# Kernel tuning notes

Hardware: AMD Instinct MI355X
Metric: run time of the kernel (lower is better)

Reference implementation:

```python
import jax, jax.numpy as jnp
import numpy as np
import math

R, C, B, E = 64, 256, 1, 768
H, DK, F = 8, 96, 3072
EPS = 1e-5


def _ln(x, w, b):
    m = jnp.mean(x, axis=-1, keepdims=True)
    v = jnp.var(x, axis=-1, keepdims=True)
    return (x - m) / jnp.sqrt(v + EPS) * w + b


def _lin(x, w, b):
    # torch Linear: y = x @ W^T + b, W: [out, in]
    return jnp.einsum('...i,oi->...o', x, w) + b


def setup_inputs() -> dict:
    key = jax.random.key(0)
    ks = jax.random.split(key, 16)
    w = lambda k, s: jax.random.normal(k, s, dtype=jnp.float32) * 0.02
    z = lambda s: jnp.zeros(s, dtype=jnp.float32)
    o = lambda s: jnp.ones(s, dtype=jnp.float32)
    return {
        'x': jax.random.normal(ks[0], (R, C, B, E), dtype=jnp.float32),
        'ln_row_w': o((E,)), 'ln_row_b': z((E,)),
        'row_q_w': w(ks[1], (E, E)), 'row_q_b': z((E,)),
        'row_k_w': w(ks[2], (E, E)), 'row_k_b': z((E,)),
        'row_v_w': w(ks[3], (E, E)), 'row_v_b': z((E,)),
        'row_o_w': w(ks[4], (E, E)), 'row_o_b': z((E,)),
        'ln_col_w': o((E,)), 'ln_col_b': z((E,)),
        'col_q_w': w(ks[5], (E, E)), 'col_q_b': z((E,)),
        'col_k_w': w(ks[6], (E, E)), 'col_k_b': z((E,)),
        'col_v_w': w(ks[7], (E, E)), 'col_v_b': z((E,)),
        'col_o_w': w(ks[8], (E, E)), 'col_o_b': z((E,)),
        'ln_ffn_w': o((E,)), 'ln_ffn_b': z((E,)),
        'fc1_w': w(ks[9], (F, E)), 'fc1_b': z((F,)),
        'fc2_w': w(ks[10], (E, F)), 'fc2_b': z((E,)),
    }


def reference(x, ln_row_w, ln_row_b, row_q_w, row_q_b, row_k_w, row_k_b,
              row_v_w, row_v_b, row_o_w, row_o_b,
              ln_col_w, ln_col_b, col_q_w, col_q_b, col_k_w, col_k_b,
              col_v_w, col_v_b, col_o_w, col_o_b,
              ln_ffn_w, ln_ffn_b, fc1_w, fc1_b, fc2_w, fc2_b):
    r, c, n, e = x.shape  # n_rows, n_cols, batch, embed

    # ---- Row self-attention (pre-LN residual block) ----
    xn = _ln(x, ln_row_w, ln_row_b)
    scaling = (DK ** -0.5) / math.sqrt(r)  # align_scaling: extra 1/sqrt(n_rows)
    q = _lin(xn, row_q_w, row_q_b).reshape(r, c, n, H, DK) * scaling
    k = _lin(xn, row_k_w, row_k_b).reshape(r, c, n, H, DK)
    v = _lin(xn, row_v_w, row_v_b).reshape(r, c, n, H, DK)
    row_logits = jnp.einsum('rinhd,rjnhd->hnij', q, k)  # sums over rows
    row_probs = jax.nn.softmax(row_logits, axis=-1)     # [H, B, C, C]
    rc = jnp.einsum('hnij,rjnhd->rinhd', row_probs, v).reshape(r, c, n, e)
    x = x + _lin(rc, row_o_w, row_o_b)

    # ---- Column self-attention (pre-LN residual block) ----
    xn = _ln(x, ln_col_w, ln_col_b)
    q = _lin(xn, col_q_w, col_q_b).reshape(r, c, n, H, DK) * (DK ** -0.5)
    k = _lin(xn, col_k_w, col_k_b).reshape(r, c, n, H, DK)
    v = _lin(xn, col_v_w, col_v_b).reshape(r, c, n, H, DK)
    col_logits = jnp.einsum('icnhd,jcnhd->hcnij', q, k)
    col_probs = jax.nn.softmax(col_logits, axis=-1)     # [H, C, B, R, R]
    cc = jnp.einsum('hcnij,jcnhd->icnhd', col_probs, v).reshape(r, c, n, e)
    x = x + _lin(cc, col_o_w, col_o_b)

    # ---- Feed-forward (pre-LN residual block) ----
    xn = _ln(x, ln_ffn_w, ln_ffn_b)
    h = jax.nn.gelu(_lin(xn, fc1_w, fc1_b), approximate=False)
    x = x + _lin(h, fc2_w, fc2_b)

    return x, row_probs, col_probs
```

## Files before the change

### kernel.cpp

```cpp
#include <hip/hip_runtime.h>
#include <cstdint>

typedef unsigned short u16;
typedef __attribute__((ext_vector_type(8))) short short8;
typedef __attribute__((ext_vector_type(4))) short short4v;
typedef __attribute__((ext_vector_type(4))) float floatx4;

#define DEV __device__ __forceinline__

DEV float bf2f(u16 u) { union { uint32_t i; float f; } w; w.i = ((uint32_t)u) << 16; return w.f; }
DEV u16 f2bf(float f) {
  union { float f; uint32_t i; } w; w.f = f;
  uint32_t x = w.i;
  return (u16)((x + 0x7fffu + ((x >> 16) & 1u)) >> 16);
}

DEV float fast_gelu(float x) {
  const float y = x * 0.70710678118f;
  const float ay = fabsf(y);
  const float t = 1.f / (1.f + 0.3275911f * ay);
  const float poly = t * (0.254829592f + t * (-0.284496736f +
                     t * (1.421413741f + t * (-1.453152027f + t * 1.061405429f))));
  const float er = 1.f - poly * __expf(-y * y);
  const float erf_y = __builtin_copysignf(er, y);
  return 0.5f * x * (1.f + erf_y);
}

DEV void async_copy16(const u16* g, u16* l) {
  __builtin_amdgcn_global_load_lds(
      (const __attribute__((address_space(1))) void*)(uintptr_t)g,
      (__attribute__((address_space(3))) void*)(uint32_t)(uintptr_t)l,
      16, 0, 0);
}

struct CvtArgs {
  const float* src[10];
  float scale[10];
};
__global__ __launch_bounds__(256) void cvt_all(CvtArgs a, u16* __restrict__ dst) {
  const size_t e = ((size_t)blockIdx.x * 256 + threadIdx.x) * 4;
  if (e >= 9437184) return;
  int reg;
  size_t base;
  if (e < 4718592) { reg = (int)(e / 589824); base = (size_t)reg * 589824; }
  else if (e < 7077888) { reg = 8; base = 4718592; }
  else { reg = 9; base = 7077888; }
  const float sc = a.scale[reg];
  floatx4 f = *(const floatx4*)(a.src[reg] + (e - base));
  short4v o;
#pragma unroll
  for (int j = 0; j < 4; ++j) o[j] = (short)f2bf(f[j] * sc);
  *(short4v*)(dst + e) = o;
}

__global__ __launch_bounds__(256) void bias_pack(const float* __restrict__ qb,
                                                 const float* __restrict__ kb,
                                                 const float* __restrict__ vb,
                                                 float sq, float* __restrict__ out) {
  const int i = blockIdx.x * 256 + threadIdx.x;
  if (i >= 2304) return;
  const int buf = i / 768, c = i - buf * 768;
  out[i] = buf == 0 ? qb[c] * sq : (buf == 1 ? kb[c] : vb[c]);
}

template<bool INF32>
__global__ __launch_bounds__(256) void ln_kernel(const void* __restrict__ in,
                                                 const float* __restrict__ w,
                                                 const float* __restrict__ b,
                                                 u16* __restrict__ out) {
  const int wid = threadIdx.x >> 6, lane = threadIdx.x & 63;
  const int row = blockIdx.x * 4 + wid;
  const size_t base = (size_t)row * 768;
  float v[12];
#pragma unroll
  for (int p = 0; p < 3; ++p) {
    const int e = p * 256 + lane * 4;
    if constexpr (INF32) {
      floatx4 f = *(const floatx4*)((const float*)in + base + e);
#pragma unroll
      for (int j = 0; j < 4; ++j) v[p * 4 + j] = f[j];
    } else {
      short4v u = *(const short4v*)((const u16*)in + base + e);
#pragma unroll
      for (int j = 0; j < 4; ++j) v[p * 4 + j] = bf2f((u16)u[j]);
    }
  }
  float s = 0.f, sq = 0.f;
#pragma unroll
  for (int i = 0; i < 12; ++i) { s += v[i]; sq += v[i] * v[i]; }
#pragma unroll
  for (int m = 1; m < 64; m <<= 1) { s += __shfl_xor(s, m); sq += __shfl_xor(sq, m); }
  const float mean = s * (1.f / 768.f);
  const float var = sq * (1.f / 768.f) - mean * mean;
  const float rstd = rsqrtf(var + 1e-5f);
#pragma unroll
  for (int p = 0; p < 3; ++p) {
    const int e = p * 256 + lane * 4;
    floatx4 wv = *(const floatx4*)(w + e);
    floatx4 bv = *(const floatx4*)(b + e);
    short4v o;
#pragma unroll
    for (int j = 0; j < 4; ++j) {
      float y = (v[p * 4 + j] - mean) * rstd * wv[j] + bv[j];
      o[j] = (short)f2bf(y);
    }
    *(short4v*)(out + base + e) = o;
  }
}

template<int AMODE>
DEV void stage_tile(const u16* __restrict__ Ab, const u16* __restrict__ Bb,
                    int m0, int n0, int lda, int ldb, int kk0, int t,
                    u16* ldsA, u16* ldsB) {
  const int wid = t >> 6;
  const int col = (((t & 3) ^ ((t >> 2) & 3)) << 3);
#pragma unroll
  for (int i = 0; i < 2; ++i) {
    const int r = i * 64 + (t >> 2);
    const int kk = kk0 + col;
    const u16 *ga, *gb;
    if constexpr (AMODE == 0) {
      ga = Ab + (size_t)(m0 + r) * lda + kk;
      gb = Bb + (size_t)(n0 + r) * ldb + kk;
    } else {
      const int r96 = kk / 96, d = kk - r96 * 96;
      ga = Ab + (size_t)r96 * 196608 + (size_t)(m0 + r) * 768 + d;
      gb = Bb + (size_t)r96 * 196608 + (size_t)(n0 + r) * 768 + d;
    }
    async_copy16(ga, ldsA + i * 2048 + wid * 512);
    async_copy16(gb, ldsB + i * 2048 + wid * 512);
  }
}

template<int AMODE, int EPI>
__global__ __launch_bounds__(256) void gemm_bt(
    const u16* __restrict__ A, const u16* __restrict__ B,
    const float* __restrict__ bias, const void* __restrict__ res,
    void* __restrict__ out, int K, int lda, int ldb,
    long long aBatch, long long bBatch, long long outBatch, int ldc, float scale) {
  __shared__ u16 lds[3 * 8192];
  const int t = threadIdx.x;
  const int z = blockIdx.z;
  const int m0 = blockIdx.x * 128, n0 = blockIdx.y * 128;
  const u16* Ab;
  const u16* Bb;
  int koff = 0;
  if constexpr (AMODE == 0) { Ab = A + (size_t)z * aBatch; Bb = B + (size_t)z * bBatch; }
  else if constexpr (AMODE == 1) { Ab = A + z * 96; Bb = B + z * 96; }
  else { const int h = z >> 4; Ab = A + h * 96; Bb = B + h * 96; koff = (z & 15) * 384; }

  const int wid = t >> 6, lane = t & 63;
  const int wr = wid >> 1, wc = wid & 1;
  const int lrow = lane & 15, lhi = lane >> 4;
  const int swl = lrow & 3;

  floatx4 acc[4][4];
#pragma unroll
  for (int i = 0; i < 4; ++i)
#pragma unroll
    for (int j = 0; j < 4; ++j) acc[i][j] = (floatx4){0.f, 0.f, 0.f, 0.f};

  const int NT = K >> 5;

  stage_tile<AMODE>(Ab, Bb, m0, n0, lda, ldb, koff, t, lds, lds + 4096);
  if (NT > 1)
    stage_tile<AMODE>(Ab, Bb, m0, n0, lda, ldb, koff + 32, t, lds + 8192, lds + 8192 + 4096);
  if (NT > 2) asm volatile("s_waitcnt vmcnt(4)" ::: "memory");
  else        asm volatile("s_waitcnt vmcnt(0)" ::: "memory");
  __builtin_amdgcn_s_barrier();
  asm volatile("" ::: "memory");

  int cur = 0, nxt = 2;
  for (int kt = 0; kt < NT; ++kt) {
    const bool more = (kt + 2) < NT;
    if (more)
      stage_tile<AMODE>(Ab, Bb, m0, n0, lda, ldb, koff + (kt + 2) * 32, t,
                        lds + nxt * 8192, lds + nxt * 8192 + 4096);

    const u16* lA = lds + cur * 8192;
    const u16* lB = lA + 4096;
    short8 af[4], bfr[4];
#pragma unroll
    for (int mi = 0; mi < 4; ++mi)
      af[mi] = *(const short8*)&lA[(wr * 64 + mi * 16 + lrow) * 32 + ((lhi ^ swl) << 3)];
#pragma unroll
    for (int ni = 0; ni < 4; ++ni)
      bfr[ni] = *(const short8*)&lB[(wc * 64 + ni * 16 + lrow) * 32 + ((lhi ^ swl) << 3)];

    __builtin_amdgcn_s_setprio(1);
#pragma unroll
    for (int mi = 0; mi < 4; ++mi)
#pragma unroll
      for (int ni = 0; ni < 4; ++ni)
        acc[mi][ni] = __builtin_amdgcn_mfma_f32_16x16x32_bf16(af[mi], bfr[ni], acc[mi][ni], 0, 0, 0);
    __builtin_amdgcn_s_setprio(0);

    if (kt + 1 < NT) {
      if (more) asm volatile("s_waitcnt vmcnt(4)" ::: "memory");
      else      asm volatile("s_waitcnt vmcnt(0)" ::: "memory");
      __builtin_amdgcn_s_barrier();
      asm volatile("" ::: "memory");
    }
    cur = (cur == 2) ? 0 : cur + 1;
    nxt = (nxt == 2) ? 0 : nxt + 1;
  }

  const int mbase = m0 + wr * 64;
  const int nbase = n0 + wc * 64;
#pragma unroll
  for (int mi = 0; mi < 4; ++mi) {
#pragma unroll
    for (int ni = 0; ni < 4; ++ni) {
      const int n = nbase + ni * 16 + lrow;
      float bz = 0.f;
      if constexpr (EPI != 1 && EPI != 7) { if (bias) bz = bias[n]; }
#pragma unroll
      for (int r4 = 0; r4 < 4; ++r4) {
        const int m = mbase + mi * 16 + lhi * 4 + r4;
        const float val = acc[mi][ni][r4];
        if constexpr (EPI == 1) {
          ((float*)out)[(size_t)z * outBatch + (size_t)m * ldc + n] = val;
        } else if constexpr (EPI == 2) {
          ((u16*)out)[(size_t)m * ldc + n] = f2bf(fast_gelu(val + bz));
        } else if constexpr (EPI == 3) {
          const float r = ((const float*)res)[(size_t)m * ldc + n];
          ((float*)out)[(size_t)m * ldc + n] = r + val + bz;
        } else if constexpr (EPI == 4) {
          const float r = ((const float*)res)[(size_t)m * ldc + n];
          ((u16*)out)[(size_t)m * ldc + n] = f2bf(r + val + bz);
        } else if constexpr (EPI == 5) {
          const float r = bf2f(((const u16*)res)[(size_t)m * ldc + n]);
          ((float*)out)[(size_t)m * ldc + n] = r + val + bz;
        } else if constexpr (EPI == 6) {
          const float r = bf2f(((const u16*)res)[(size_t)m * ldc + n]);
          ((u16*)out)[(size_t)m * ldc + n] = f2bf(r + val + bz);
        } else if constexpr (EPI == 7) {
          const int rr = n / 96, d = n - rr * 96;
          ((u16*)out)[((size_t)(rr * 256 + m)) * 768 + (size_t)z * 96 + d] = f2bf(val);
        } else if constexpr (EPI == 8) {
          const int buf = n / 768, col = n - buf * 768;
          ((u16*)out)[(size_t)buf * 12582912 + (size_t)m * 768 + col] = f2bf(val + bz);
        }
      }
    }
  }
}

__global__ __launch_bounds__(256) void softmax_row(const float* __restrict__ part,
                                                   float* __restrict__ probs_f,
                                                   u16* __restrict__ probs_b) {
  const int wid = threadIdx.x >> 6, lane = threadIdx.x & 63;
  const int row = blockIdx.x * 4 + wid;
  const int h = row >> 8, i = row & 255;
  const size_t base = (size_t)h * 16 * 65536 + (size_t)i * 256 + lane * 4;
  floatx4 v = (floatx4){0.f, 0.f, 0.f, 0.f};
#pragma unroll
  for (int s16 = 0; s16 < 16; ++s16) {
    floatx4 p = *(const floatx4*)(part + base + (size_t)s16 * 65536);
#pragma unroll
    for (int j = 0; j < 4; ++j) v[j] += p[j];
  }
  float mx = fmaxf(fmaxf(v[0], v[1]), fmaxf(v[2], v[3]));
#pragma unroll
  for (int m = 1; m < 64; m <<= 1) mx = fmaxf(mx, __shfl_xor(mx, m));
  float e[4], s = 0.f;
#pragma unroll
  for (int j = 0; j < 4; ++j) { e[j] = __expf(v[j] - mx); s += e[j]; }
#pragma unroll
  for (int m = 1; m < 64; m <<= 1) s += __shfl_xor(s, m);
  const float inv = 1.f / s;
  floatx4 of;
  short4v ob;
#pragma unroll
  for (int j = 0; j < 4; ++j) {
    const float p = e[j] * inv;
    of[j] = p;
    ob[j] = (short)f2bf(p);
  }
  *(floatx4*)(probs_f + (size_t)row * 256 + lane * 4) = of;
  *(short4v*)(probs_b + (size_t)row * 256 + lane * 4) = ob;
}

__global__ __launch_bounds__(256) void pack_vt(const u16* __restrict__ v, u16* __restrict__ vt) {
  __shared__ u16 S[64][104];
  const int jb = blockIdx.x, r = blockIdx.y, h = blockIdx.z;
  const int t = threadIdx.x;
#pragma unroll
  for (int p = 0; p < 3; ++p) {
    const int cid = t + p * 256;
    const int j = cid / 12, ch = cid - j * 12;
    short8 x = *(const short8*)&v[((size_t)(r * 256 + jb * 64 + j)) * 768 + h * 96 + ch * 8];
    *(short8*)&S[j][ch * 8] = x;
  }
  __syncthreads();
#pragma unroll
  for (int p = 0; p < 3; ++p) {
    const int cid = t + p * 256;
    const int d = cid / 8, cj = cid - d * 8;
    u16 tmp[8];
#pragma unroll
    for (int m = 0; m < 8; ++m) tmp[m] = S[cj * 8 + m][d];
    *(short8*)&vt[((size_t)(h * 6144 + r * 96 + d)) * 256 + jb * 64 + cj * 8] = *(short8*)tmp;
  }
}

__global__ __launch_bounds__(256) void col_attn(const u16* __restrict__ q,
                                                const u16* __restrict__ k,
                                                const u16* __restrict__ v,
                                                float* __restrict__ probs,
                                                u16* __restrict__ ctx) {
  __shared__ u16 qs[64][104];
  __shared__ u16 ks[64][104];
  __shared__ u16 vt[96][72];
  __shared__ u16 ps[64][72];
  const int c = blockIdx.x, h = blockIdx.y;
  const int t = threadIdx.x;
#pragma unroll
  for (int p = 0; p < 3; ++p) {
    const int cid = t + p * 256;
    const int i = cid / 12, ch = cid - i * 12;
    const size_t g = ((size_t)(i * 256 + c)) * 768 + h * 96 + ch * 8;
    short8 qv = *(const short8*)(q + g);
    short8 kv = *(const short8*)(k + g);
    short8 vv = *(const short8*)(v + g);
    *(short8*)&qs[i][ch * 8] = qv;
    *(short8*)&ks[i][ch * 8] = kv;
#pragma unroll
    for (int m = 0; m < 8; ++m) vt[ch * 8 + m][i] = (u16)vv[m];
  }
  __syncthreads();
  const int lane = t & 63, wid = t >> 6;
  const int lrow = lane & 15, lhi = lane >> 4;

  floatx4 s[4];
#pragma unroll
  for (int nj = 0; nj < 4; ++nj) s[nj] = (floatx4){0.f, 0.f, 0.f, 0.f};
#pragma unroll
  for (int kk = 0; kk < 3; ++kk) {
    short8 a = *(const short8*)&qs[wid * 16 + lrow][kk * 32 + lhi * 8];
#pragma unroll
    for (int nj = 0; nj < 4; ++nj) {
      short8 bb = *(const short8*)&ks[nj * 16 + lrow][kk * 32 + lhi * 8];
      s[nj] = __builtin_amdgcn_mfma_f32_16x16x32_bf16(a, bb, s[nj], 0, 0, 0);
    }
  }
  const size_t pb = ((size_t)(h * 256 + c)) * 4096;
#pragma unroll
  for (int r4 = 0; r4 < 4; ++r4) {
    float mx = fmaxf(fmaxf(s[0][r4], s[1][r4]), fmaxf(s[2][r4], s[3][r4]));
    mx = fmaxf(mx, __shfl_xor(mx, 1));
    mx = fmaxf(mx, __shfl_xor(mx, 2));
    mx = fmaxf(mx, __shfl_xor(mx, 4));
    mx = fmaxf(mx, __shfl_xor(mx, 8));
    float e[4], sum = 0.f;
#pragma unroll
    for (int nj = 0; nj < 4; ++nj) { e[nj] = __expf(s[nj][r4] - mx); sum += e[nj]; }
    sum += __shfl_xor(sum, 1);
    sum += __shfl_xor(sum, 2);
    sum += __shfl_xor(sum, 4);
    sum += __shfl_xor(sum, 8);
    const float inv = 1.f / sum;
    const int i = wid * 16 + lhi * 4 + r4;
#pragma unroll
    for (int nj = 0; nj < 4; ++nj) {
      const float pv = e[nj] * inv;
      const int j = nj * 16 + lrow;
      probs[pb + (size_t)i * 64 + j] = pv;
      ps[i][j] = f2bf(pv);
    }
  }
  __syncthreads();
  floatx4 o[6];
#pragma unroll
  for (int df = 0; df < 6; ++df) o[df] = (floatx4){0.f, 0.f, 0.f, 0.f};
#pragma unroll
  for (int k2 = 0; k2 < 2; ++k2) {
    short8 a = *(const short8*)&ps[wid * 16 + lrow][k2 * 32 + lhi * 8];
#pragma unroll
    for (int df = 0; df < 6; ++df) {
      short8 bb = *(const short8*)&vt[df * 16 + lrow][k2 * 32 + lhi * 8];
      o[df] = __builtin_amdgcn_mfma_f32_16x16x32_bf16(a, bb, o[df], 0, 0, 0);
    }
  }
#pragma unroll
  for (int df = 0; df < 6; ++df)
#pragma unroll
    for (int r4 = 0; r4 < 4; ++r4) {
      const int i = wid * 16 + lhi * 4 + r4;
      const int d = df * 16 + lrow;
      ctx[((size_t)(i * 256 + c)) * 768 + h * 96 + d] = f2bf(o[df][r4]);
    }
}

extern "C" void kernel_launch(void* const* d_in, const int* in_sizes, int n_in,
                              void* d_out, int out_size, void* d_ws, size_t ws_size,
                              hipStream_t stream) {
  const float* x_in  = (const float*)d_in[0];
  const float* lnr_w = (const float*)d_in[1];
  const float* lnr_b = (const float*)d_in[2];
  const float* rq_w  = (const float*)d_in[3];
  const float* rq_b  = (const float*)d_in[4];
  const float* rk_w  = (const float*)d_in[5];
  const float* rk_b  = (const float*)d_in[6];
  const float* rv_w  = (const float*)d_in[7];
  const float* rv_b  = (const float*)d_in[8];
  const float* ro_w  = (const float*)d_in[9];
  const float* ro_b  = (const float*)d_in[10];
  const float* lnc_w = (const float*)d_in[11];
  const float* lnc_b = (const float*)d_in[12];
  const float* cq_w  = (const float*)d_in[13];
  const float* cq_b  = (const float*)d_in[14];
  const float* ck_w  = (const float*)d_in[15];
  const float* ck_b  = (const float*)d_in[16];
  const float* cv_w  = (const float*)d_in[17];
  const float* cv_b  = (const float*)d_in[18];
  const float* co_w  = (const float*)d_in[19];
  const float* co_b  = (const float*)d_in[20];
  const float* lnf_w = (const float*)d_in[21];
  const float* lnf_b = (const float*)d_in[22];
  const float* f1_w  = (const float*)d_in[23];
  const float* f1_b  = (const float*)d_in[24];
  const float* f2_w  = (const float*)d_in[25];
  const float* f2_b  = (const float*)d_in[26];

  const float s_row = 0.0127577591f;
  const float s_col = 0.1020620726f;

  char* ws = (char*)d_ws;
  const size_t WSZ_E = 589824 * 2;
  u16* w_all = (u16*)ws;
  u16* w_rqkv = w_all;
  u16* w_ro   = (u16*)(ws + 3 * WSZ_E);
  u16* w_cqkv = (u16*)(ws + 4 * WSZ_E);
  u16* w_co   = (u16*)(ws + 7 * WSZ_E);
  u16* w_f1   = (u16*)(ws + 8 * WSZ_E);
  u16* w_f2   = (u16*)(ws + 8 * WSZ_E + 4718592);
  size_t off = 8 * WSZ_E + 2 * 4718592;

  const bool xf32 = ws_size >= 147849216ULL;
  char* x_cur = ws + off;
  off += xf32 ? 50331648 : 25165824;
  u16* qb = (u16*)(ws + off); off += 25165824;
  u16* kb = (u16*)(ws + off); off += 25165824;
  u16* vb = (u16*)(ws + off); off += 25165824;
  u16* probsb = (u16*)(ws + off); off += 1048576;
  float* qkvb_row = (float*)(ws + off); off += 9216;
  float* qkvb_col = (float*)(ws + off); off += 9216;

  u16* vt     = qb;
  u16* ctx1   = kb;
  u16* hidden = qb;
  u16* xn3    = vb;

  float* out_x  = (float*)d_out;
  float* out_rp = out_x + 12582912;
  float* out_cp = out_x + 13107200;
  u16* xn   = (u16*)out_x;
  u16* ctx2 = (u16*)((char*)out_x + 25165824);
  float* part = out_x;

  const dim3 blk(256);

  CvtArgs ca;
  ca.src[0] = rq_w; ca.src[1] = rk_w; ca.src[2] = rv_w; ca.src[3] = ro_w;
  ca.src[4] = cq_w; ca.src[5] = ck_w; ca.src[6] = cv_w; ca.src[7] = co_w;
  ca.src[8] = f1_w; ca.src[9] = f2_w;
  for (int i = 0; i < 10; ++i) ca.scale[i] = 1.f;
  ca.scale[0] = s_row; ca.scale[4] = s_col;
  cvt_all<<<9216, blk, 0, stream>>>(ca, w_all);
  bias_pack<<<9, blk, 0, stream>>>(rq_b, rk_b, rv_b, s_row, qkvb_row);
  bias_pack<<<9, blk, 0, stream>>>(cq_b, ck_b, cv_b, s_col, qkvb_col);

  ln_kernel<true><<<4096, blk, 0, stream>>>(x_in, lnr_w, lnr_b, xn);
  gemm_bt<0, 8><<<dim3(128, 18, 1), blk, 0, stream>>>(xn, w_rqkv, qkvb_row, nullptr, qb, 768, 768, 768, 0, 0, 0, 768, 1.f);
  gemm_bt<2, 1><<<dim3(2, 2, 128), blk, 0, stream>>>(qb, kb, nullptr, nullptr, part, 384, 0, 0, 0, 0, 65536LL, 256, 1.f);
  softmax_row<<<512, blk, 0, stream>>>(part, out_rp, probsb);
  pack_vt<<<dim3(4, 64, 8), blk, 0, stream>>>(vb, vt);
  gemm_bt<0, 7><<<dim3(2, 48, 8), blk, 0, stream>>>(probsb, vt, nullptr, nullptr, ctx1, 256, 256, 256, 65536LL, 1572864LL, 0, 0, 1.f);
  if (xf32)
    gemm_bt<0, 3><<<dim3(128, 6, 1), blk, 0, stream>>>(ctx1, w_ro, ro_b, x_in, x_cur, 768, 768, 768, 0, 0, 0, 768, 1.f);
  else
    gemm_bt<0, 4><<<dim3(128, 6, 1), blk, 0, stream>>>(ctx1, w_ro, ro_b, x_in, x_cur, 768, 768, 768, 0, 0, 0, 768, 1.f);

  if (xf32) ln_kernel<true><<<4096, blk, 0, stream>>>(x_cur, lnc_w, lnc_b, xn);
  else      ln_kernel<false><<<4096, blk, 0, stream>>>(x_cur, lnc_w, lnc_b, xn);
  gemm_bt<0, 8><<<dim3(128, 18, 1), blk, 0, stream>>>(xn, w_cqkv, qkvb_col, nullptr, qb, 768, 768, 768, 0, 0, 0, 768, 1.f);
  col_attn<<<dim3(256, 8), blk, 0, stream>>>(qb, kb, vb, out_cp, ctx2);
  if (xf32)
    gemm_bt<0, 3><<<dim3(128, 6, 1), blk, 0, stream>>>(ctx2, w_co, co_b, x_cur, x_cur, 768, 768, 768, 0, 0, 0, 768, 1.f);
  else
    gemm_bt<0, 6><<<dim3(128, 6, 1), blk, 0, stream>>>(ctx2, w_co, co_b, x_cur, x_cur, 768, 768, 768, 0, 0, 0, 768, 1.f);

  if (xf32) ln_kernel<true><<<4096, blk, 0, stream>>>(x_cur, lnf_w, lnf_b, xn3);
  else      ln_kernel<false><<<4096, blk, 0, stream>>>(x_cur, lnf_w, lnf_b, xn3);
  gemm_bt<0, 2><<<dim3(128, 12, 1), blk, 0, stream>>>(xn3, w_f1, f1_b, nullptr, hidden, 768, 768, 768, 0, 0, 0, 1536, 1.f);
  if (xf32)
    gemm_bt<0, 3><<<dim3(128, 6, 1), blk, 0, stream>>>(hidden, w_f2, f2_b, x_cur, out_x, 1536, 1536, 3072, 0, 0, 0, 768, 1.f);
  else
    gemm_bt<0, 5><<<dim3(128, 6, 1), blk, 0, stream>>>(hidden, w_f2, f2_b, x_cur, out_x, 1536, 1536, 3072, 0, 0, 0, 768, 1.f);
  gemm_bt<0, 2><<<dim3(128, 12, 1), blk, 0, stream>>>(xn3, w_f1 + 1536 * 768, f1_b + 1536, nullptr, hidden, 768, 768, 768, 0, 0, 0, 1536, 1.f);
  gemm_bt<0, 3><<<dim3(128, 6, 1), blk, 0, stream>>>(hidden, w_f2 + 1536, nullptr, out_x, out_x, 1536, 1536, 3072, 0, 0, 0, 768, 1.f);
}
```

Measured before the change: 620.1 us.

## Pre-pack GEMM B operands into tile-contiguous layout for coalesced LDS staging

Weights and the transposed V buffer are now written in a blocked layout of 128x32 tiles, with the 8-element k-chunks laid out contiguously. The GEMM gains a BP template mode that stages B with one fully contiguous 16-byte load per lane and reads fragments without swizzling. The goal is better global-load coalescing and fewer LDS bank conflicts on the B side. In exchange, the weight conversion kernel now reads with a strided gather, and the ldb argument is reinterpreted as a count of k-tiles per row.

Result: no change. 618.9 us (-0.2%).

```diff
diff --git a/kernel.cpp b/kernel.cpp
--- a/kernel.cpp
+++ b/kernel.cpp
@@ -40,16 +40,23 @@
 __global__ __launch_bounds__(256) void cvt_all(CvtArgs a, u16* __restrict__ dst) {
   const size_t e = ((size_t)blockIdx.x * 256 + threadIdx.x) * 4;
   if (e >= 9437184) return;
-  int reg;
+  int reg, N, K;
   size_t base;
-  if (e < 4718592) { reg = (int)(e / 589824); base = (size_t)reg * 589824; }
-  else if (e < 7077888) { reg = 8; base = 4718592; }
-  else { reg = 9; base = 7077888; }
+  if (e < 4718592) { reg = (int)(e / 589824); base = (size_t)reg * 589824; N = 768; K = 768; }
+  else if (e < 7077888) { reg = 8; base = 4718592; N = 3072; K = 768; }
+  else { reg = 9; base = 7077888; N = 768; K = 3072; }
+  const int NKT = K >> 5;
+  const size_t r = e - base;
+  const int tile = (int)(r >> 12);
+  const int nt = tile / NKT, kt = tile - nt * NKT;
+  const int rem = (int)(r & 4095);
+  const int c = rem >> 10, row = (rem >> 3) & 127, j = rem & 7;
+  const int n = nt * 128 + row, k = kt * 32 + c * 8 + j;
   const float sc = a.scale[reg];
-  floatx4 f = *(const floatx4*)(a.src[reg] + (e - base));
+  floatx4 f = *(const floatx4*)(a.src[reg] + (size_t)n * K + k);
   short4v o;
 #pragma unroll
-  for (int j = 0; j < 4; ++j) o[j] = (short)f2bf(f[j] * sc);
+  for (int q = 0; q < 4; ++q) o[q] = (short)f2bf(f[q] * sc);
   *(short4v*)(dst + e) = o;
 }
 
@@ -108,36 +115,49 @@
   }
 }
 
-template<int AMODE>
-DEV void stage_tile(const u16* __restrict__ Ab, const u16* __restrict__ Bb,
-                    int m0, int n0, int lda, int ldb, int kk0, int t,
+template<int AMODE, int BP>
+DEV void stage_tile(const u16* __restrict__ Ab, const u16* __restrict__ Bsrc,
+                    int m0, int n0, int lda, int ldb, int kk0, int ktAbs, int t,
                     u16* ldsA, u16* ldsB) {
-  const int wid = t >> 6;
+  const int wid = t >> 6, lane = t & 63;
   const int col = (((t & 3) ^ ((t >> 2) & 3)) << 3);
 #pragma unroll
   for (int i = 0; i < 2; ++i) {
     const int r = i * 64 + (t >> 2);
     const int kk = kk0 + col;
-    const u16 *ga, *gb;
+    const u16* ga;
     if constexpr (AMODE == 0) {
       ga = Ab + (size_t)(m0 + r) * lda + kk;
-      gb = Bb + (size_t)(n0 + r) * ldb + kk;
     } else {
       const int r96 = kk / 96, d = kk - r96 * 96;
       ga = Ab + (size_t)r96 * 196608 + (size_t)(m0 + r) * 768 + d;
-      gb = Bb + (size_t)r96 * 196608 + (size_t)(n0 + r) * 768 + d;
     }
     async_copy16(ga, ldsA + i * 2048 + wid * 512);
-    async_copy16(gb, ldsB + i * 2048 + wid * 512);
-  }
-}
-
-template<int AMODE, int EPI>
+
+    const int slot = i * 4 + wid;
+    if constexpr (BP) {
+      const u16* gb = Bsrc + (size_t)ktAbs * 4096 + slot * 512 + lane * 8;
+      async_copy16(gb, ldsB + slot * 512);
+    } else {
+      const u16* gb;
+      if constexpr (AMODE == 0) {
+        gb = Bsrc + (size_t)(n0 + r) * ldb + kk;
+      } else {
+        const int r96 = kk / 96, d = kk - r96 * 96;
+        gb = Bsrc + (size_t)r96 * 196608 + (size_t)(n0 + r) * 768 + d;
+      }
+      async_copy16(gb, ldsB + i * 2048 + wid * 512);
+    }
+  }
+}
+
+template<int AMODE, int EPI, int BP>
 __global__ __launch_bounds__(256) void gemm_bt(
     const u16* __restrict__ A, const u16* __restrict__ B,
     const float* __restrict__ bias, const void* __restrict__ res,
     void* __restrict__ out, int K, int lda, int ldb,
-    long long aBatch, long long bBatch, long long outBatch, int ldc, float scale) {
+    long long aBatch, long long bBatch, long long outBatch, int ldc, int bkt0,
+    float scale) {
   __shared__ u16 lds[3 * 8192];
   const int t = threadIdx.x;
   const int z = blockIdx.z;
@@ -146,8 +166,11 @@
   const u16* Bb;
   int koff = 0;
   if constexpr (AMODE == 0) { Ab = A + (size_t)z * aBatch; Bb = B + (size_t)z * bBatch; }
-  else if constexpr (AMODE == 1) { Ab = A + z * 96; Bb = B + z * 96; }
   else { const int h = z >> 4; Ab = A + h * 96; Bb = B + h * 96; koff = (z & 15) * 384; }
+
+  const u16* Bstage;
+  if constexpr (BP) Bstage = Bb + ((size_t)((n0 >> 7) * ldb + bkt0)) * 4096;
+  else Bstage = Bb;
 
   const int wid = t >> 6, lane = t & 63;
   const int wr = wid >> 1, wc = wid & 1;
@@ -162,9 +185,10 @@
 
   const int NT = K >> 5;
 
-  stage_tile<AMODE>(Ab, Bb, m0, n0, lda, ldb, koff, t, lds, lds + 4096);
+  stage_tile<AMODE, BP>(Ab, Bstage, m0, n0, lda, ldb, koff, 0, t, lds, lds + 4096);
   if (NT > 1)
-    stage_tile<AMODE>(Ab, Bb, m0, n0, lda, ldb, koff + 32, t, lds + 8192, lds + 8192 + 4096);
+    stage_tile<AMODE, BP>(Ab, Bstage, m0, n0, lda, ldb, koff + 32, 1, t,
+                          lds + 8192, lds + 8192 + 4096);
   if (NT > 2) asm volatile("s_waitcnt vmcnt(4)" ::: "memory");
   else        asm volatile("s_waitcnt vmcnt(0)" ::: "memory");
   __builtin_amdgcn_s_barrier();
@@ -174,8 +198,8 @@
   for (int kt = 0; kt < NT; ++kt) {
     const bool more = (kt + 2) < NT;
     if (more)
-      stage_tile<AMODE>(Ab, Bb, m0, n0, lda, ldb, koff + (kt + 2) * 32, t,
-                        lds + nxt * 8192, lds + nxt * 8192 + 4096);
+      stage_tile<AMODE, BP>(Ab, Bstage, m0, n0, lda, ldb, koff + (kt + 2) * 32, kt + 2, t,
+                            lds + nxt * 8192, lds + nxt * 8192 + 4096);
 
     const u16* lA = lds + cur * 8192;
     const u16* lB = lA + 4096;
@@ -184,8 +208,12 @@
     for (int mi = 0; mi < 4; ++mi)
       af[mi] = *(const short8*)&lA[(wr * 64 + mi * 16 + lrow) * 32 + ((lhi ^ swl) << 3)];
 #pragma unroll
-    for (int ni = 0; ni < 4; ++ni)
-      bfr[ni] = *(const short8*)&lB[(wc * 64 + ni * 16 + lrow) * 32 + ((lhi ^ swl) << 3)];
+    for (int ni = 0; ni < 4; ++ni) {
+      if constexpr (BP)
+        bfr[ni] = *(const short8*)&lB[lhi * 1024 + (wc * 64 + ni * 16 + lrow) * 8];
+      else
+        bfr[ni] = *(const short8*)&lB[(wc * 64 + ni * 16 + lrow) * 32 + ((lhi ^ swl) << 3)];
+    }
 
     __builtin_amdgcn_s_setprio(1);
 #pragma unroll
@@ -300,7 +328,12 @@
     u16 tmp[8];
 #pragma unroll
     for (int m = 0; m < 8; ++m) tmp[m] = S[cj * 8 + m][d];
-    *(short8*)&vt[((size_t)(h * 6144 + r * 96 + d)) * 256 + jb * 64 + cj * 8] = *(short8*)tmp;
+    const int row_t = r * 96 + d;
+    const int k = jb * 64 + cj * 8;
+    const size_t off = (size_t)h * 1572864 +
+                       ((size_t)((row_t >> 7) * 8 + (k >> 5))) * 4096 +
+                       ((k >> 3) & 3) * 1024 + (row_t & 127) * 8;
+    *(short8*)&vt[off] = *(short8*)tmp;
   }
 }
 
@@ -472,32 +505,32 @@
   bias_pack<<<9, blk, 0, stream>>>(cq_b, ck_b, cv_b, s_col, qkvb_col);
 
   ln_kernel<true><<<4096, blk, 0, stream>>>(x_in, lnr_w, lnr_b, xn);
-  gemm_bt<0, 8><<<dim3(128, 18, 1), blk, 0, stream>>>(xn, w_rqkv, qkvb_row, nullptr, qb, 768, 768, 768, 0, 0, 0, 768, 1.f);
-  gemm_bt<2, 1><<<dim3(2, 2, 128), blk, 0, stream>>>(qb, kb, nullptr, nullptr, part, 384, 0, 0, 0, 0, 65536LL, 256, 1.f);
+  gemm_bt<0, 8, 1><<<dim3(128, 18, 1), blk, 0, stream>>>(xn, w_rqkv, qkvb_row, nullptr, qb, 768, 768, 24, 0, 0, 0, 768, 0, 1.f);
+  gemm_bt<2, 1, 0><<<dim3(2, 2, 128), blk, 0, stream>>>(qb, kb, nullptr, nullptr, part, 384, 0, 0, 0, 0, 65536LL, 256, 0, 1.f);
   softmax_row<<<512, blk, 0, stream>>>(part, out_rp, probsb);
   pack_vt<<<dim3(4, 64, 8), blk, 0, stream>>>(vb, vt);
-  gemm_bt<0, 7><<<dim3(2, 48, 8), blk, 0, stream>>>(probsb, vt, nullptr, nullptr, ctx1, 256, 256, 256, 65536LL, 1572864LL, 0, 0, 1.f);
+  gemm_bt<0, 7, 1><<<dim3(2, 48, 8), blk, 0, stream>>>(probsb, vt, nullptr, nullptr, ctx1, 256, 256, 8, 65536LL, 1572864LL, 0, 0, 0, 1.f);
   if (xf32)
-    gemm_bt<0, 3><<<dim3(128, 6, 1), blk, 0, stream>>>(ctx1, w_ro, ro_b, x_in, x_cur, 768, 768, 768, 0, 0, 0, 768, 1.f);
+    gemm_bt<0, 3, 1><<<dim3(128, 6, 1), blk, 0, stream>>>(ctx1, w_ro, ro_b, x_in, x_cur, 768, 768, 24, 0, 0, 0, 768, 0, 1.f);
   else
-    gemm_bt<0, 4><<<dim3(128, 6, 1), blk, 0, stream>>>(ctx1, w_ro, ro_b, x_in, x_cur, 768, 768, 768, 0, 0, 0, 768, 1.f);
+    gemm_bt<0, 4, 1><<<dim3(128, 6, 1), blk, 0, stream>>>(ctx1, w_ro, ro_b, x_in, x_cur, 768, 768, 24, 0, 0, 0, 768, 0, 1.f);
 
   if (xf32) ln_kernel<true><<<4096, blk, 0, stream>>>(x_cur, lnc_w, lnc_b, xn);
   else      ln_kernel<false><<<4096, blk, 0, stream>>>(x_cur, lnc_w, lnc_b, xn);
-  gemm_bt<0, 8><<<dim3(128, 18, 1), blk, 0, stream>>>(xn, w_cqkv, qkvb_col, nullptr, qb, 768, 768, 768, 0, 0, 0, 768, 1.f);
+  gemm_bt<0, 8, 1><<<dim3(128, 18, 1), blk, 0, stream>>>(xn, w_cqkv, qkvb_col, nullptr, qb, 768, 768, 24, 0, 0, 0, 768, 0, 1.f);
   col_attn<<<dim3(256, 8), blk, 0, stream>>>(qb, kb, vb, out_cp, ctx2);
   if (xf32)
-    gemm_bt<0, 3><<<dim3(128, 6, 1), blk, 0, stream>>>(ctx2, w_co, co_b, x_cur, x_cur, 768, 768, 768, 0, 0, 0, 768, 1.f);
+    gemm_bt<0, 3, 1><<<dim3(128, 6, 1), blk, 0, stream>>>(ctx2, w_co, co_b, x_cur, x_cur, 768, 768, 24, 0, 0, 0, 768, 0, 1.f);
   else
-    gemm_bt<0, 6><<<dim3(128, 6, 1), blk, 0, stream>>>(ctx2, w_co, co_b, x_cur, x_cur, 768, 768, 768, 0, 0, 0, 768, 1.f);
+    gemm_bt<0, 6, 1><<<dim3(128, 6, 1), blk, 0, stream>>>(ctx2, w_co, co_b, x_cur, x_cur, 768, 768, 24, 0, 0, 0, 768, 0, 1.f);
 
   if (xf32) ln_kernel<true><<<4096, blk, 0, stream>>>(x_cur, lnf_w, lnf_b, xn3);
   else      ln_kernel<false><<<4096, blk, 0, stream>>>(x_cur, lnf_w, lnf_b, xn3);
-  gemm_bt<0, 2><<<dim3(128, 12, 1), blk, 0, stream>>>(xn3, w_f1, f1_b, nullptr, hidden, 768, 768, 768, 0, 0, 0, 1536, 1.f);
+  gemm_bt<0, 2, 1><<<dim3(128, 12, 1), blk, 0, stream>>>(xn3, w_f1, f1_b, nullptr, hidden, 768, 768, 24, 0, 0, 0, 1536, 0, 1.f);
   if (xf32)
-    gemm_bt<0, 3><<<dim3(128, 6, 1), blk, 0, stream>>>(hidden, w_f2, f2_b, x_cur, out_x, 1536, 1536, 3072, 0, 0, 0, 768, 1.f);
+    gemm_bt<0, 3, 1><<<dim3(128, 6, 1), blk, 0, stream>>>(hidden, w_f2, f2_b, x_cur, out_x, 1536, 1536, 96, 0, 0, 0, 768, 0, 1.f);
   else
-    gemm_bt<0, 5><<<dim3(128, 6, 1), blk, 0, stream>>>(hidden, w_f2, f2_b, x_cur, out_x, 1536, 1536, 3072, 0, 0, 0, 768, 1.f);
-  gemm_bt<0, 2><<<dim3(128, 12, 1), blk, 0, stream>>>(xn3, w_f1 + 1536 * 768, f1_b + 1536, nullptr, hidden, 768, 768, 768, 0, 0, 0, 1536, 1.f);
-  gemm_bt<0, 3><<<dim3(128, 6, 1), blk, 0, stream>>>(hidden, w_f2 + 1536, nullptr, out_x, out_x, 1536, 1536, 3072, 0, 0, 0, 768, 1.f);
-}
+    gemm_bt<0, 5, 1><<<dim3(128, 6, 1), blk, 0, stream>>>(hidden, w_f2, f2_b, x_cur, out_x, 1536, 1536, 96, 0, 0, 0, 768, 0, 1.f);
+  gemm_bt<0, 2, 1><<<dim3(128, 12, 1), blk, 0, stream>>>(xn3, w_f1 + 1536 * 768, f1_b + 1536, nullptr, hidden, 768, 768, 24, 0, 0, 0, 1536, 0, 1.f);
+  gemm_bt<0, 3, 1><<<dim3(128, 6, 1), blk, 0, stream>>>(hidden, w_f2, nullptr, out_x, out_x, 1536, 1536, 96, 0, 0, 0, 768, 48, 1.f);
+}
```
